# Optimization experiments

Measured on AMD Instinct MI355X. Metric: run time of the kernel, lower is better.

Reference implementation:

```python
import jax, jax.numpy as jnp
import numpy as np


def setup_inputs() -> dict:
    key = jax.random.key(0)
    ks = jax.random.split(key, 5)
    B, S, H = 64, 1024, 1024
    scale = 1.0 / np.sqrt(H)
    return {
        "decoder_hidden": jax.random.normal(ks[0], (B, H), jnp.float32),
        "encoder_outputs": jax.random.normal(ks[1], (B, S, H), jnp.float32),
        "W1": jax.random.normal(ks[2], (H, H), jnp.float32) * scale,
        "W2": jax.random.normal(ks[3], (H, H), jnp.float32) * scale,
        "v": jax.random.normal(ks[4], (H,), jnp.float32) * scale,
    }


def reference(decoder_hidden, encoder_outputs, W1, W2, v):
    # W1 @ decoder_hidden: [B, H] computed once, broadcast over src_len
    dh_proj = jnp.einsum("bh,oh->bo", decoder_hidden, W1)          # [B, H]
    enc_proj = jnp.einsum("bsh,oh->bso", encoder_outputs, W2)      # [B, S, H]
    energy = jnp.tanh(dh_proj[:, None, :] + enc_proj)              # [B, S, H]
    scores = jnp.einsum("bsh,h->bs", energy, v)                    # [B, S]
    attention_weights = jax.nn.softmax(scores, axis=-1)            # [B, S]
    context = jnp.einsum("bs,bsh->bh", attention_weights, encoder_outputs)
    return (context, attention_weights)
```

## Files before the change

### kernel.cpp

```cpp
#include <hip/hip_runtime.h>
#include <hip/hip_bf16.h>
#include <cmath>

#define Hdim 1024
#define Bdim 64
#define Sdim 1024

typedef __attribute__((ext_vector_type(4))) float f32x4;
typedef __attribute__((ext_vector_type(8))) short s16x8;
typedef __attribute__((ext_vector_type(4))) unsigned int u32x4;

static __device__ __forceinline__ unsigned short f2bf(float f) {
  unsigned int u = __builtin_bit_cast(unsigned int, f);
  unsigned int r = (u + 0x7fffu + ((u >> 16) & 1u)) >> 16;
  return (unsigned short)r;
}

static __device__ __forceinline__ float bf2f(unsigned short u) {
  return __builtin_bit_cast(float, (unsigned int)u << 16);
}

#define TANH_C 2.885390081777927f


static __device__ __forceinline__ void stage_rows64(const float* __restrict__ src,
                                                    unsigned short* As, int tid) {
  #pragma unroll 4
  for (int i = 0; i < 32; ++i) {
    int c = tid + i * 256;
    int row = c >> 7;
    int k8 = (c & 127) << 3;
    const float4* p = reinterpret_cast<const float4*>(src + row * Hdim + k8);
    float4 a = p[0];
    float4 b = p[1];
    union { unsigned short us[8]; u32x4 v; } pk;
    pk.us[0] = f2bf(a.x); pk.us[1] = f2bf(a.y); pk.us[2] = f2bf(a.z); pk.us[3] = f2bf(a.w);
    pk.us[4] = f2bf(b.x); pk.us[5] = f2bf(b.y); pk.us[6] = f2bf(b.z); pk.us[7] = f2bf(b.w);
    int idx = row * Hdim + (k8 ^ ((row & 7) << 3));
    *reinterpret_cast<u32x4*>(&As[idx]) = pk.v;
  }
}

static __device__ __forceinline__ s16x8 lda_full(const unsigned short* As, int row, int k) {
  int idx = row * Hdim + (k ^ ((row & 7) << 3));
  return *reinterpret_cast<const s16x8*>(&As[idx]);
}

static __device__ __forceinline__ s16x8 ldb_g(const unsigned short* __restrict__ Wb,
                                              const float* __restrict__ Wf,
                                              int use_bf, int o, int k) {
  if (use_bf) {
    return *reinterpret_cast<const s16x8*>(&Wb[o * Hdim + k]);
  } else {
    const float4* p = reinterpret_cast<const float4*>(Wf + o * Hdim + k);
    float4 a = p[0];
    float4 b = p[1];
    union { unsigned short us[8]; s16x8 v; } pk;
    pk.us[0] = f2bf(a.x); pk.us[1] = f2bf(a.y); pk.us[2] = f2bf(a.z); pk.us[3] = f2bf(a.w);
    pk.us[4] = f2bf(b.x); pk.us[5] = f2bf(b.y); pk.us[6] = f2bf(b.z); pk.us[7] = f2bf(b.w);
    return pk.v;
  }
}

__global__ void cast_bf16_kernel(const float* __restrict__ src,
                                 unsigned short* __restrict__ dst) {
  int i = blockIdx.x * 256 + threadIdx.x;
  const float4* p = reinterpret_cast<const float4*>(src) + i * 2;
  float4 a = p[0];
  float4 b = p[1];
  union { unsigned short us[8]; u32x4 v; } pk;
  pk.us[0] = f2bf(a.x); pk.us[1] = f2bf(a.y); pk.us[2] = f2bf(a.z); pk.us[3] = f2bf(a.w);
  pk.us[4] = f2bf(b.x); pk.us[5] = f2bf(b.y); pk.us[6] = f2bf(b.z); pk.us[7] = f2bf(b.w);
  *reinterpret_cast<u32x4*>(dst + i * 8) = pk.v;
}

__global__ __launch_bounds__(256, 1) void proj_kernel(
    const float* __restrict__ dh, const float* __restrict__ W1f,
    const unsigned short* __restrict__ W1b, float* __restrict__ out, int use_bf) {
  __shared__ unsigned short As[64 * Hdim];
  int tid = threadIdx.x;
  stage_rows64(dh, As, tid);
  __syncthreads();
  int w = tid >> 6, lane = tid & 63;
  int lo = lane & 15, hi = lane >> 4;
  int o = blockIdx.x * 16 + lo;
  f32x4 acc = {0.f, 0.f, 0.f, 0.f};
  for (int k0 = 0; k0 < Hdim; k0 += 32) {
    int k = k0 + hi * 8;
    s16x8 bfrag = ldb_g(W1b, W1f, use_bf, o, k);
    s16x8 afrag = lda_full(As, w * 16 + lo, k);
    acc = __builtin_amdgcn_mfma_f32_16x16x32_bf16(afrag, bfrag, acc, 0, 0, 0);
  }
  #pragma unroll
  for (int r = 0; r < 4; ++r)
    out[(w * 16 + hi * 4 + r) * Hdim + o] = acc[r];
}

#define SBM 256
#define SBN 256
#define SBK 64

__global__ __launch_bounds__(512, 2) void score_mfma_kernel(
    const unsigned short* __restrict__ encb,
    const unsigned short* __restrict__ W2b,
    const float* __restrict__ dhp, const float* __restrict__ v,
    float* __restrict__ scores) {
  __shared__ unsigned short As[2][SBM * SBK];
  __shared__ unsigned short Bs[2][SBN * SBK];
  __shared__ float ssum[SBM];
  int tid = threadIdx.x;
  int bid = blockIdx.x;
  int swz = (bid & 7) * 128 + (bid >> 3);
  int mp = swz >> 2;
  int np = swz & 3;
  int row0 = mp * SBM;
  int b = row0 >> 10;
  int w = tid >> 6, lane = tid & 63;
  int wr = w >> 2, wc = w & 3;
  int lo = lane & 15, hi = lane >> 4;

  if (tid < SBM) ssum[tid] = 0.f;

  const unsigned short* gA[4];
  const unsigned short* gB[4];
  #pragma unroll
  for (int i = 0; i < 4; ++i) {
    int d = i * 512 + tid;
    int row = d >> 3, c = d & 7;
    int gc = c ^ (row & 7);
    gA[i] = encb + (size_t)(row0 + row) * Hdim + gc * 8;
    gB[i] = W2b + (size_t)(np * SBN + row) * Hdim + gc * 8;
  }

  auto STAGE = [&](int buf) {
    #pragma unroll
    for (int i = 0; i < 4; ++i) {
      int dwv = i * 512 + w * 64;
      __builtin_amdgcn_global_load_lds(
          (const __attribute__((address_space(1))) unsigned int*)gA[i],
          (__attribute__((address_space(3))) unsigned int*)(&As[buf][dwv * 8]), 16, 0, 0);
      __builtin_amdgcn_global_load_lds(
          (const __attribute__((address_space(1))) unsigned int*)gB[i],
          (__attribute__((address_space(3))) unsigned int*)(&Bs[buf][dwv * 8]), 16, 0, 0);
      gA[i] += SBK;
      gB[i] += SBK;
    }
  };

  f32x4 acc[8][4] = {};

  STAGE(0);
  asm volatile("s_waitcnt vmcnt(0)" ::: "memory");
  __syncthreads();

  int cur = 0;
  for (int t = 0; t < 16; ++t) {
    if (t < 15) STAGE(cur ^ 1);

    const char* Ab = (const char*)As[cur];
    const char* Bb = (const char*)Bs[cur];
    #pragma unroll
    for (int ks = 0; ks < 2; ++ks) {
      int kb = (ks * 32 + hi * 8) * 2;
      s16x8 af[8], bf[4];
      #pragma unroll
      for (int m = 0; m < 8; ++m) {
        int row = wr * 128 + m * 16 + lo;
        af[m] = *reinterpret_cast<const s16x8*>(Ab + row * (SBK * 2) + (kb ^ ((row & 7) << 4)));
      }
      #pragma unroll
      for (int n = 0; n < 4; ++n) {
        int row = wc * 64 + n * 16 + lo;
        bf[n] = *reinterpret_cast<const s16x8*>(Bb + row * (SBK * 2) + (kb ^ ((row & 7) << 4)));
      }
      #pragma unroll
      for (int m = 0; m < 8; ++m)
        #pragma unroll
        for (int n = 0; n < 4; ++n)
          acc[m][n] = __builtin_amdgcn_mfma_f32_16x16x32_bf16(af[m], bf[n], acc[m][n], 0, 0, 0);
    }
    asm volatile("s_waitcnt vmcnt(0)" ::: "memory");
    __syncthreads();
    cur ^= 1;
  }

  float psum[8][4] = {};
  #pragma unroll
  for (int n = 0; n < 4; ++n) {
    int o = np * SBN + wc * 64 + n * 16 + lo;
    float dv = dhp[b * Hdim + o];
    float vv = v[o];
    float vv2 = 2.f * vv;
    #pragma unroll
    for (int m = 0; m < 8; ++m)
      #pragma unroll
      for (int r = 0; r < 4; ++r) {
        float x = acc[m][n][r] + dv;
        float e2 = __builtin_amdgcn_exp2f(x * TANH_C);
        float rc = __builtin_amdgcn_rcpf(1.f + e2);
        psum[m][r] += vv - vv2 * rc;
      }
  }
  #pragma unroll
  for (int mask = 1; mask < 16; mask <<= 1)
    #pragma unroll
    for (int m = 0; m < 8; ++m)
      #pragma unroll
      for (int r = 0; r < 4; ++r)
        psum[m][r] += __shfl_xor(psum[m][r], mask, 64);
  if (lo == 0) {
    #pragma unroll
    for (int m = 0; m < 8; ++m)
      #pragma unroll
      for (int r = 0; r < 4; ++r)
        atomicAdd(&ssum[wr * 128 + m * 16 + hi * 4 + r], psum[m][r]);
  }
  __syncthreads();
  if (tid < SBM) atomicAdd(&scores[row0 + tid], ssum[tid]);
}

#define BKt 64

__global__ __launch_bounds__(256, 3) void score_kernel(
    const float* __restrict__ enc, const float* __restrict__ W2f,
    const unsigned short* __restrict__ W2b, const float* __restrict__ dhp,
    const float* __restrict__ v, float* __restrict__ scores, int use_bf) {
  __shared__ unsigned short As[64 * BKt];
  int tid = threadIdx.x;
  int bid = blockIdx.x;
  int f = (bid & 7) * 512 + (bid >> 3);
  int rg = f >> 2;
  int oc = f & 3;
  int row0 = rg * 64;
  int b = row0 >> 10;
  int w = tid >> 6, lane = tid & 63;
  int lo = lane & 15, hi = lane >> 4;
  int n0 = oc * 256 + w * 64;

  const unsigned short* pB[4];
  const float* pBf[4];
  #pragma unroll
  for (int n = 0; n < 4; ++n) {
    int o = n0 + n * 16 + lo;
    pB[n]  = W2b + (size_t)o * Hdim + hi * 8;
    pBf[n] = W2f + (size_t)o * Hdim + hi * 8;
  }

  f32x4 acc[4][4] = {};

  for (int t = 0; t < 16; ++t) {
    int k0 = t * BKt;
    __syncthreads();
    #pragma unroll
    for (int cc = 0; cc < 2; ++cc) {
      int c = tid + cc * 256;
      int row = c >> 3;
      int j = c & 7;
      const float4* p = reinterpret_cast<const float4*>(
          enc + (size_t)(row0 + row) * Hdim + k0 + j * 8);
      float4 a = p[0];
      float4 bb = p[1];
      union { unsigned short us[8]; u32x4 v4; } pk;
      pk.us[0] = f2bf(a.x);  pk.us[1] = f2bf(a.y);  pk.us[2] = f2bf(a.z);  pk.us[3] = f2bf(a.w);
      pk.us[4] = f2bf(bb.x); pk.us[5] = f2bf(bb.y); pk.us[6] = f2bf(bb.z); pk.us[7] = f2bf(bb.w);
      int idx = row * BKt + ((j * 8) ^ ((row & 7) << 3));
      *reinterpret_cast<u32x4*>(&As[idx]) = pk.v4;
    }
    __syncthreads();

    #pragma unroll
    for (int ks = 0; ks < 2; ++ks) {
      s16x8 bfrag[4];
      #pragma unroll
      for (int n = 0; n < 4; ++n) {
        if (use_bf) {
          bfrag[n] = *reinterpret_cast<const s16x8*>(pB[n] + ks * 32);
        } else {
          const float4* p = reinterpret_cast<const float4*>(pBf[n] + ks * 32);
          float4 a = p[0];
          float4 bb = p[1];
          union { unsigned short us[8]; s16x8 v4; } pk;
          pk.us[0] = f2bf(a.x);  pk.us[1] = f2bf(a.y);  pk.us[2] = f2bf(a.z);  pk.us[3] = f2bf(a.w);
          pk.us[4] = f2bf(bb.x); pk.us[5] = f2bf(bb.y); pk.us[6] = f2bf(bb.z); pk.us[7] = f2bf(bb.w);
          bfrag[n] = pk.v4;
        }
      }
      #pragma unroll
      for (int m = 0; m < 4; ++m) {
        int kk = ks * 32 + hi * 8;
        s16x8 afrag = *reinterpret_cast<const s16x8*>(
            &As[(m * 16 + lo) * BKt + (kk ^ ((lo & 7) << 3))]);
        #pragma unroll
        for (int n = 0; n < 4; ++n)
          acc[m][n] = __builtin_amdgcn_mfma_f32_16x16x32_bf16(afrag, bfrag[n], acc[m][n], 0, 0, 0);
      }
    }
    #pragma unroll
    for (int n = 0; n < 4; ++n) { pB[n] += BKt; pBf[n] += BKt; }
  }

  float psum[4][4] = {};
  #pragma unroll
  for (int n = 0; n < 4; ++n) {
    int o = n0 + n * 16 + lo;
    float dv = dhp[b * Hdim + o];
    float vv = v[o];
    float vv2 = 2.f * vv;
    #pragma unroll
    for (int m = 0; m < 4; ++m)
      #pragma unroll
      for (int r = 0; r < 4; ++r) {
        float x = acc[m][n][r] + dv;
        float e2 = __builtin_amdgcn_exp2f(x * TANH_C);
        float rc = __builtin_amdgcn_rcpf(1.f + e2);
        psum[m][r] += vv - vv2 * rc;
      }
  }
  #pragma unroll
  for (int mask = 1; mask < 16; mask <<= 1)
    #pragma unroll
    for (int m = 0; m < 4; ++m)
      #pragma unroll
      for (int r = 0; r < 4; ++r)
        psum[m][r] += __shfl_xor(psum[m][r], mask, 64);
  if (lo == 0) {
    #pragma unroll
    for (int m = 0; m < 4; ++m)
      #pragma unroll
      for (int r = 0; r < 4; ++r)
        atomicAdd(&scores[row0 + m * 16 + hi * 4 + r], psum[m][r]);
  }
}

__global__ __launch_bounds__(256, 1) void softmax_kernel(float* __restrict__ attn) {
  __shared__ float redm[4];
  __shared__ float reds[4];
  int b = blockIdx.x, tid = threadIdx.x;
  float4 x = *reinterpret_cast<float4*>(attn + b * Sdim + tid * 4);
  float m = fmaxf(fmaxf(x.x, x.y), fmaxf(x.z, x.w));
  #pragma unroll
  for (int mask = 1; mask < 64; mask <<= 1) m = fmaxf(m, __shfl_xor(m, mask, 64));
  if ((tid & 63) == 0) redm[tid >> 6] = m;
  __syncthreads();
  m = fmaxf(fmaxf(redm[0], redm[1]), fmaxf(redm[2], redm[3]));
  float4 e;
  e.x = expf(x.x - m); e.y = expf(x.y - m); e.z = expf(x.z - m); e.w = expf(x.w - m);
  float s = e.x + e.y + e.z + e.w;
  #pragma unroll
  for (int mask = 1; mask < 64; mask <<= 1) s += __shfl_xor(s, mask, 64);
  if ((tid & 63) == 0) reds[tid >> 6] = s;
  __syncthreads();
  s = reds[0] + reds[1] + reds[2] + reds[3];
  float inv = 1.f / s;
  e.x *= inv; e.y *= inv; e.z *= inv; e.w *= inv;
  *reinterpret_cast<float4*>(attn + b * Sdim + tid * 4) = e;
}

__global__ __launch_bounds__(256, 1) void context_bf_kernel(
    const unsigned short* __restrict__ encb, const float* __restrict__ attn,
    float* __restrict__ ctx) {
  int b = blockIdx.x >> 4;
  int chunk = blockIdx.x & 15;
  int tid = threadIdx.x;
  int h0 = tid * 4;
  const unsigned short* ebase = encb + ((size_t)(b * Sdim + chunk * 64)) * Hdim + h0;
  const float* abase = attn + b * Sdim + chunk * 64;
  float4 acc = {0.f, 0.f, 0.f, 0.f};
  #pragma unroll 4
  for (int s = 0; s < 64; ++s) {
    float wgt = abase[s];
    ushort4 ev = *reinterpret_cast<const ushort4*>(ebase + (size_t)s * Hdim);
    acc.x += wgt * bf2f(ev.x);
    acc.y += wgt * bf2f(ev.y);
    acc.z += wgt * bf2f(ev.z);
    acc.w += wgt * bf2f(ev.w);
  }
  float* c = ctx + b * Hdim + h0;
  atomicAdd(c + 0, acc.x);
  atomicAdd(c + 1, acc.y);
  atomicAdd(c + 2, acc.z);
  atomicAdd(c + 3, acc.w);
}

__global__ __launch_bounds__(256, 1) void context_kernel(
    const float* __restrict__ enc, const float* __restrict__ attn,
    float* __restrict__ ctx) {
  int b = blockIdx.x >> 3;
  int chunk = blockIdx.x & 7;
  int tid = threadIdx.x;
  int h0 = tid * 4;
  const float* ebase = enc + ((size_t)(b * Sdim + chunk * 128)) * Hdim + h0;
  const float* abase = attn + b * Sdim + chunk * 128;
  float4 acc = {0.f, 0.f, 0.f, 0.f};
  #pragma unroll 4
  for (int s = 0; s < 128; ++s) {
    float wgt = abase[s];
    float4 ev = *reinterpret_cast<const float4*>(ebase + (size_t)s * Hdim);
    acc.x += wgt * ev.x; acc.y += wgt * ev.y; acc.z += wgt * ev.z; acc.w += wgt * ev.w;
  }
  float* c = ctx + b * Hdim + h0;
  atomicAdd(c + 0, acc.x);
  atomicAdd(c + 1, acc.y);
  atomicAdd(c + 2, acc.z);
  atomicAdd(c + 3, acc.w);
}

extern "C" void kernel_launch(void* const* d_in, const int* in_sizes, int n_in,
                              void* d_out, int out_size, void* d_ws, size_t ws_size,
                              hipStream_t stream) {
  const float* dh  = (const float*)d_in[0];
  const float* enc = (const float*)d_in[1];
  const float* W1  = (const float*)d_in[2];
  const float* W2  = (const float*)d_in[3];
  const float* v   = (const float*)d_in[4];
  float* out_ctx  = (float*)d_out;
  float* out_attn = out_ctx + Bdim * Hdim;

  int use_bf = (ws_size >= 4ull * 1024 * 1024) ? 1 : 0;
  int big_ws = (ws_size >= 133ull * 1024 * 1024) ? 1 : 0;
  unsigned short* W1b  = (unsigned short*)d_ws;
  unsigned short* W2b  = W1b + 1024 * 1024;
  unsigned short* encb = W2b + 1024 * 1024;

  if (use_bf) {
    cast_bf16_kernel<<<512, 256, 0, stream>>>(W1, W1b);
    cast_bf16_kernel<<<512, 256, 0, stream>>>(W2, W2b);
  }
  if (big_ws) {
    cast_bf16_kernel<<<32768, 256, 0, stream>>>(enc, encb);
  }

  proj_kernel<<<64, 256, 0, stream>>>(dh, W1, W1b, out_ctx, use_bf);

  hipMemsetAsync(out_attn, 0, (size_t)Bdim * Sdim * sizeof(float), stream);
  if (big_ws) {
    score_mfma_kernel<<<1024, 512, 0, stream>>>(encb, W2b, out_ctx, v, out_attn);
  } else {
    score_kernel<<<4096, 256, 0, stream>>>(enc, W2, W2b, out_ctx, v, out_attn, use_bf);
  }

  softmax_kernel<<<Bdim, 256, 0, stream>>>(out_attn);

  hipMemsetAsync(out_ctx, 0, (size_t)Bdim * Hdim * sizeof(float), stream);
  if (big_ws) {
    context_bf_kernel<<<1024, 256, 0, stream>>>(encb, out_attn, out_ctx);
  } else {
    context_kernel<<<512, 256, 0, stream>>>(enc, out_attn, out_ctx);
  }
}
```

Measured before the change: 297.9 us.

## Triple-buffer A tiles with partial vmcnt waits and direct global atomics

```diff
diff --git a/kernel.cpp b/kernel.cpp
--- a/kernel.cpp
+++ b/kernel.cpp
@@ -105,9 +105,8 @@
     const unsigned short* __restrict__ W2b,
     const float* __restrict__ dhp, const float* __restrict__ v,
     float* __restrict__ scores) {
-  __shared__ unsigned short As[2][SBM * SBK];
+  __shared__ unsigned short As[3][SBM * SBK];
   __shared__ unsigned short Bs[2][SBN * SBK];
-  __shared__ float ssum[SBM];
   int tid = threadIdx.x;
   int bid = blockIdx.x;
   int swz = (bid & 7) * 128 + (bid >> 3);
@@ -119,8 +118,6 @@
   int wr = w >> 2, wc = w & 3;
   int lo = lane & 15, hi = lane >> 4;
 
-  if (tid < SBM) ssum[tid] = 0.f;
-
   const unsigned short* gA[4];
   const unsigned short* gB[4];
   #pragma unroll
@@ -132,46 +129,57 @@
     gB[i] = W2b + (size_t)(np * SBN + row) * Hdim + gc * 8;
   }
 
-  auto STAGE = [&](int buf) {
+  auto STAGE_A = [&](int t, int s) {
     #pragma unroll
     for (int i = 0; i < 4; ++i) {
       int dwv = i * 512 + w * 64;
       __builtin_amdgcn_global_load_lds(
-          (const __attribute__((address_space(1))) unsigned int*)gA[i],
-          (__attribute__((address_space(3))) unsigned int*)(&As[buf][dwv * 8]), 16, 0, 0);
+          (const __attribute__((address_space(1))) unsigned int*)(gA[i] + t * SBK),
+          (__attribute__((address_space(3))) unsigned int*)(&As[s][dwv * 8]), 16, 0, 0);
+    }
+  };
+  auto STAGE_B = [&](int t, int s) {
+    #pragma unroll
+    for (int i = 0; i < 4; ++i) {
+      int dwv = i * 512 + w * 64;
       __builtin_amdgcn_global_load_lds(
-          (const __attribute__((address_space(1))) unsigned int*)gB[i],
-          (__attribute__((address_space(3))) unsigned int*)(&Bs[buf][dwv * 8]), 16, 0, 0);
-      gA[i] += SBK;
-      gB[i] += SBK;
+          (const __attribute__((address_space(1))) unsigned int*)(gB[i] + t * SBK),
+          (__attribute__((address_space(3))) unsigned int*)(&Bs[s][dwv * 8]), 16, 0, 0);
     }
   };
 
   f32x4 acc[8][4] = {};
 
-  STAGE(0);
-  asm volatile("s_waitcnt vmcnt(0)" ::: "memory");
-  __syncthreads();
-
-  int cur = 0;
+  STAGE_A(0, 0); STAGE_B(0, 0);
+  STAGE_A(1, 1); STAGE_B(1, 1);
+  STAGE_A(2, 2);
+  asm volatile("s_waitcnt vmcnt(12)" ::: "memory");
+  __builtin_amdgcn_s_barrier();
+  asm volatile("" ::: "memory");
+
+  int xorA = (lo & 7) << 4;
+
+  #pragma unroll
   for (int t = 0; t < 16; ++t) {
-    if (t < 15) STAGE(cur ^ 1);
-
-    const char* Ab = (const char*)As[cur];
-    const char* Bb = (const char*)Bs[cur];
+    if (t >= 1 && t + 1 < 16) STAGE_B(t + 1, (t + 1) & 1);
+    if (t >= 1 && t + 2 < 16) STAGE_A(t + 2, (t + 2) % 3);
+
+    const char* Ab = (const char*)As[t % 3];
+    const char* Bb = (const char*)Bs[t & 1];
+    __builtin_amdgcn_s_setprio(1);
     #pragma unroll
     for (int ks = 0; ks < 2; ++ks) {
-      int kb = (ks * 32 + hi * 8) * 2;
+      int kb = ks * 64 + hi * 16;
       s16x8 af[8], bf[4];
       #pragma unroll
       for (int m = 0; m < 8; ++m) {
         int row = wr * 128 + m * 16 + lo;
-        af[m] = *reinterpret_cast<const s16x8*>(Ab + row * (SBK * 2) + (kb ^ ((row & 7) << 4)));
+        af[m] = *reinterpret_cast<const s16x8*>(Ab + row * 128 + (kb ^ xorA));
       }
       #pragma unroll
       for (int n = 0; n < 4; ++n) {
         int row = wc * 64 + n * 16 + lo;
-        bf[n] = *reinterpret_cast<const s16x8*>(Bb + row * (SBK * 2) + (kb ^ ((row & 7) << 4)));
+        bf[n] = *reinterpret_cast<const s16x8*>(Bb + row * 128 + (kb ^ xorA));
       }
       #pragma unroll
       for (int m = 0; m < 8; ++m)
@@ -179,9 +187,14 @@
         for (int n = 0; n < 4; ++n)
           acc[m][n] = __builtin_amdgcn_mfma_f32_16x16x32_bf16(af[m], bf[n], acc[m][n], 0, 0, 0);
     }
-    asm volatile("s_waitcnt vmcnt(0)" ::: "memory");
-    __syncthreads();
-    cur ^= 1;
+    __builtin_amdgcn_s_setprio(0);
+    if (t <= 13) {
+      asm volatile("s_waitcnt vmcnt(4)" ::: "memory");
+    } else {
+      asm volatile("s_waitcnt vmcnt(0)" ::: "memory");
+    }
+    __builtin_amdgcn_s_barrier();
+    asm volatile("" ::: "memory");
   }
 
   float psum[8][4] = {};
@@ -213,10 +226,8 @@
     for (int m = 0; m < 8; ++m)
       #pragma unroll
       for (int r = 0; r < 4; ++r)
-        atomicAdd(&ssum[wr * 128 + m * 16 + hi * 4 + r], psum[m][r]);
-  }
-  __syncthreads();
-  if (tid < SBM) atomicAdd(&scores[row0 + tid], ssum[tid]);
+        atomicAdd(&scores[row0 + wr * 128 + m * 16 + hi * 4 + r], psum[m][r]);
+  }
 }
 
 #define BKt 64
```

Result: no change. 303.0 us (+1.7%).
